# Kernel optimization log

Hardware: AMD Instinct MI355X
Metric: run time of the kernel (lower is better)

Reference implementation:

```python
import jax, jax.numpy as jnp
import numpy as np

N = 4096      # num_nodes
F = 256       # node_dim
K = 4         # num_heads
FP = 64       # out_dim per head
P_EDGE = 0.008  # edge probability (~33 avg degree)


def setup_inputs() -> dict:
    key = jax.random.key(0)
    k1, k2, k3, k4, k5 = jax.random.split(key, 5)
    x = jax.random.normal(k1, (N, F), dtype=jnp.float32)
    # binary adjacency mask with self loops so every row has a neighbor
    adj = (jax.random.uniform(k2, (N, N)) < P_EDGE).astype(jnp.float32)
    mask = jnp.maximum(adj, jnp.eye(N, dtype=jnp.float32))
    batch = jnp.zeros((N,), dtype=jnp.int32)  # unused (is_final_layer=False)
    # xavier-style init for W (node_dim -> K*FP) and attention vectors
    w_scale = np.sqrt(2.0 / (F + K * FP)).astype(np.float32)
    W = jax.random.normal(k3, (F, K * FP), dtype=jnp.float32) * w_scale
    b = jnp.zeros((K * FP,), dtype=jnp.float32)
    a_scale = np.sqrt(2.0 / (K * FP + 1)).astype(np.float32)
    a_left = jax.random.normal(k4, (1, K, FP), dtype=jnp.float32) * a_scale
    a_right = jax.random.normal(k5, (1, K, FP), dtype=jnp.float32) * a_scale
    return {"x": x, "mask": mask, "batch": batch, "W": W, "b": b,
            "a_left": a_left, "a_right": a_right}


def reference(x, mask, batch, W, b, a_left, a_right):
    # dropout prob = 0.0 (eval mode) -> identity
    x_proj = (x @ W + b).reshape(N, K, FP)                 # (N,K,F')
    score_src = (x_proj * a_left).sum(axis=-1)             # (N,K)
    score_tgt = (x_proj * a_right).sum(axis=-1)            # (N,K)
    score = score_src[:, None, :] + score_tgt[None, :, :]  # (N,N,K)
    score = jax.nn.leaky_relu(score, negative_slope=0.2)
    # non-standard global mean/std normalization (torch .std() is unbiased)
    score = (score - score.mean()) / score.std(ddof=1)
    score = jnp.exp(score)
    m = mask[:, :, None]                                   # (N,N,1)
    denom = (score * m).sum(axis=1, keepdims=True)         # (N,1,K)
    aij = (score / denom) * m                              # (N,N,K)
    attention = jnp.transpose(aij, (2, 0, 1))              # (K,N,N)
    h_prime = jnp.einsum('knm,mkf->nkf', attention, x_proj)  # (N,K,F')
    h_prime = jax.nn.elu(h_prime)
    # is_final_layer=False -> concat heads
    return h_prime.reshape(N, K * FP)
```

## Files before the change

kernel.cpp:

```cpp
#include <hip/hip_runtime.h>
#include <hip/hip_bf16.h>
#include <math.h>

#define NN 4096
#define FF 256
#define KH 4
#define FP 64
#define NCOL 256
#define MAXNBR 512
#define GEMM_BLKS 512
#define MOM_BLOCKS 4096

__device__ __forceinline__ float bits2f(unsigned b) {
    union { unsigned u; float f; } c; c.u = b << 16; return c.f;
}
__device__ __forceinline__ int is_fp32(const void* mask) {
    return ((const unsigned*)mask)[0] == 0x3F800000u;
}

#define OFF_PART   0
#define OFF_MUSIG  65536
#define OFF_XP     131072
#define OFF_SRC    4325376
#define OFF_TGT    4390912
#define OFF_NBR    4456448
#define OFF_CNT    8650752

__global__ __launch_bounds__(256) void k_gemm_scan(
        const void* __restrict__ xr, const void* __restrict__ mask,
        const void* __restrict__ Wr, const void* __restrict__ br,
        const void* __restrict__ alr, const void* __restrict__ arr,
        float* __restrict__ xp, float* __restrict__ srcb, float* __restrict__ tgtb,
        unsigned short* __restrict__ nbr_g, int* __restrict__ cnt_g) {
    const int fl = is_fp32(mask);
    const int tid = threadIdx.x;
    __shared__ union {
        float4 xs[8][64];
        struct { unsigned short snbr[MAXNBR]; int cnt; } sc;
    } sm;

    if (blockIdx.x >= GEMM_BLKS) {
        int n = blockIdx.x - GEMM_BLKS;
        if (tid == 0) sm.sc.cnt = 0;
        __syncthreads();
        if (fl) {
            const uint4* p = (const uint4*)((const float*)mask + (size_t)n * NN);
            for (int i = tid; i < NN / 4; i += 256) {
                uint4 v = p[i]; int base = i * 4;
                if (v.x) { int s = atomicAdd(&sm.sc.cnt, 1); if (s < MAXNBR) sm.sc.snbr[s] = base + 0; }
                if (v.y) { int s = atomicAdd(&sm.sc.cnt, 1); if (s < MAXNBR) sm.sc.snbr[s] = base + 1; }
                if (v.z) { int s = atomicAdd(&sm.sc.cnt, 1); if (s < MAXNBR) sm.sc.snbr[s] = base + 2; }
                if (v.w) { int s = atomicAdd(&sm.sc.cnt, 1); if (s < MAXNBR) sm.sc.snbr[s] = base + 3; }
            }
        } else {
            const uint4* p = (const uint4*)((const unsigned short*)mask + (size_t)n * NN);
            for (int i = tid; i < NN / 8; i += 256) {
                uint4 v = p[i]; int base = i * 8;
                if (v.x & 0xFFFFu) { int s = atomicAdd(&sm.sc.cnt, 1); if (s < MAXNBR) sm.sc.snbr[s] = base + 0; }
                if (v.x >> 16)     { int s = atomicAdd(&sm.sc.cnt, 1); if (s < MAXNBR) sm.sc.snbr[s] = base + 1; }
                if (v.y & 0xFFFFu) { int s = atomicAdd(&sm.sc.cnt, 1); if (s < MAXNBR) sm.sc.snbr[s] = base + 2; }
                if (v.y >> 16)     { int s = atomicAdd(&sm.sc.cnt, 1); if (s < MAXNBR) sm.sc.snbr[s] = base + 3; }
                if (v.z & 0xFFFFu) { int s = atomicAdd(&sm.sc.cnt, 1); if (s < MAXNBR) sm.sc.snbr[s] = base + 4; }
                if (v.z >> 16)     { int s = atomicAdd(&sm.sc.cnt, 1); if (s < MAXNBR) sm.sc.snbr[s] = base + 5; }
                if (v.w & 0xFFFFu) { int s = atomicAdd(&sm.sc.cnt, 1); if (s < MAXNBR) sm.sc.snbr[s] = base + 6; }
                if (v.w >> 16)     { int s = atomicAdd(&sm.sc.cnt, 1); if (s < MAXNBR) sm.sc.snbr[s] = base + 7; }
            }
        }
        __syncthreads();
        int c = sm.sc.cnt < MAXNBR ? sm.sc.cnt : MAXNBR;
        for (int j = tid; j < c; j += 256)
            nbr_g[(size_t)n * MAXNBR + j] = sm.sc.snbr[j];
        if (tid == 0) cnt_g[n] = c;
        return;
    }

    int n0 = blockIdx.x * 8;
    if (fl) {
        const float4* xq = (const float4*)xr;
        for (int t = tid; t < 512; t += 256) {
            int r = t >> 6, q = t & 63;
            sm.xs[r][q] = xq[(size_t)(n0 + r) * 64 + q];
        }
    } else {
        const ushort4* xq = (const ushort4*)xr;
        for (int t = tid; t < 512; t += 256) {
            int r = t >> 6, q = t & 63;
            ushort4 u = xq[(size_t)(n0 + r) * 64 + q];
            float4 v; v.x = bits2f(u.x); v.y = bits2f(u.y); v.z = bits2f(u.z); v.w = bits2f(u.w);
            sm.xs[r][q] = v;
        }
    }
    __syncthreads();
    int c = tid;
    float acc[8] = {};
    if (fl) {
        const float* WF = (const float*)Wr;
        for (int kk = 0; kk < 64; ++kk) {
            float w0 = WF[(4 * kk + 0) * NCOL + c];
            float w1 = WF[(4 * kk + 1) * NCOL + c];
            float w2 = WF[(4 * kk + 2) * NCOL + c];
            float w3 = WF[(4 * kk + 3) * NCOL + c];
            #pragma unroll
            for (int r = 0; r < 8; ++r) {
                float4 xv = sm.xs[r][kk];
                acc[r] += xv.x * w0 + xv.y * w1 + xv.z * w2 + xv.w * w3;
            }
        }
    } else {
        const unsigned short* WB = (const unsigned short*)Wr;
        for (int kk = 0; kk < 64; ++kk) {
            float w0 = bits2f(WB[(4 * kk + 0) * NCOL + c]);
            float w1 = bits2f(WB[(4 * kk + 1) * NCOL + c]);
            float w2 = bits2f(WB[(4 * kk + 2) * NCOL + c]);
            float w3 = bits2f(WB[(4 * kk + 3) * NCOL + c]);
            #pragma unroll
            for (int r = 0; r < 8; ++r) {
                float4 xv = sm.xs[r][kk];
                acc[r] += xv.x * w0 + xv.y * w1 + xv.z * w2 + xv.w * w3;
            }
        }
    }
    float bv, alv, arv;
    if (fl) {
        bv  = ((const float*)br)[c];
        alv = ((const float*)alr)[c];
        arv = ((const float*)arr)[c];
    } else {
        bv  = bits2f(((const unsigned short*)br)[c]);
        alv = bits2f(((const unsigned short*)alr)[c]);
        arv = bits2f(((const unsigned short*)arr)[c]);
    }
    int wave = tid >> 6;
    int lane = tid & 63;
    #pragma unroll
    for (int r = 0; r < 8; ++r) {
        float o = acc[r] + bv;
        xp[(size_t)(n0 + r) * NCOL + c] = o;
        float sr = o * alv, tr = o * arv;
        #pragma unroll
        for (int off = 32; off; off >>= 1) {
            sr += __shfl_down(sr, off, 64);
            tr += __shfl_down(tr, off, 64);
        }
        if (lane == 0) {
            srcb[(n0 + r) * KH + wave] = sr;
            tgtb[(n0 + r) * KH + wave] = tr;
        }
    }
}

__global__ __launch_bounds__(256) void k_moments(
        const float* __restrict__ srcb, const float* __restrict__ tgtb,
        double2* __restrict__ partials) {
    const int total = NN * NN;
    const int stride = MOM_BLOCKS * 256;
    float s1 = 0.f, s2 = 0.f;
    #pragma unroll 4
    for (int p = blockIdx.x * 256 + threadIdx.x; p < total; p += stride) {
        int n = p >> 12, m = p & 4095;
        float4 sv = ((const float4*)srcb)[n];
        float4 tv = ((const float4*)tgtb)[m];
        float v0 = sv.x + tv.x; v0 = v0 > 0.f ? v0 : 0.2f * v0;
        float v1 = sv.y + tv.y; v1 = v1 > 0.f ? v1 : 0.2f * v1;
        float v2 = sv.z + tv.z; v2 = v2 > 0.f ? v2 : 0.2f * v2;
        float v3 = sv.w + tv.w; v3 = v3 > 0.f ? v3 : 0.2f * v3;
        s1 += v0 + v1 + v2 + v3;
        s2 += v0 * v0 + v1 * v1 + v2 * v2 + v3 * v3;
    }
    __shared__ double l1[256], l2[256];
    l1[threadIdx.x] = (double)s1;
    l2[threadIdx.x] = (double)s2;
    __syncthreads();
    for (int off = 128; off; off >>= 1) {
        if (threadIdx.x < off) {
            l1[threadIdx.x] += l1[threadIdx.x + off];
            l2[threadIdx.x] += l2[threadIdx.x + off];
        }
        __syncthreads();
    }
    if (threadIdx.x == 0) {
        double2 pr; pr.x = l1[0]; pr.y = l2[0];
        partials[blockIdx.x] = pr;
    }
}

__global__ __launch_bounds__(256) void k_fold(
        const double2* __restrict__ partials, float* __restrict__ musig) {
    double a = 0.0, b2 = 0.0;
    for (int i = threadIdx.x; i < MOM_BLOCKS; i += 256) {
        double2 pr = partials[i];
        a += pr.x; b2 += pr.y;
    }
    __shared__ double l1[256], l2[256];
    l1[threadIdx.x] = a;
    l2[threadIdx.x] = b2;
    __syncthreads();
    for (int off = 128; off; off >>= 1) {
        if (threadIdx.x < off) {
            l1[threadIdx.x] += l1[threadIdx.x + off];
            l2[threadIdx.x] += l2[threadIdx.x + off];
        }
        __syncthreads();
    }
    if (threadIdx.x == 0) {
        double s = l1[0], ss = l2[0];
        const double tot = (double)NN * (double)NN * (double)KH;
        musig[0] = (float)(s / tot);
        musig[1] = (float)(1.0 / sqrt((ss - s * s / tot) / (tot - 1.0)));
    }
}

__global__ __launch_bounds__(256) void k_aggregate(
        const unsigned short* __restrict__ nbr_g, const int* __restrict__ cnt_g,
        const float* __restrict__ musig,
        const float* __restrict__ xp,
        const float* __restrict__ srcb, const float* __restrict__ tgtb,
        float* __restrict__ out) {
    const int tid = threadIdx.x;
    __shared__ unsigned short snbr[MAXNBR];
    __shared__ float pls[MAXNBR * KH];
    __shared__ float invden[KH];
    float mu = musig[0], inv_sigma = musig[1];
    int n = blockIdx.x;
    int c = cnt_g[n];
    for (int j = tid; j < c; j += 256) snbr[j] = nbr_g[(size_t)n * MAXNBR + j];
    __syncthreads();

    for (int t = tid; t < c * KH; t += 256) {
        int j = t >> 2, k = t & 3;
        int m = snbr[j];
        float v = srcb[n * KH + k] + tgtb[m * KH + k];
        v = v > 0.f ? v : 0.2f * v;
        pls[j * KH + k] = expf((v - mu) * inv_sigma);
    }
    __syncthreads();
    if (tid < KH) {
        float d = 0.f;
        for (int j = 0; j < c; ++j) d += pls[j * KH + tid];
        invden[tid] = 1.0f / d;
    }
    __syncthreads();

    int col = tid;
    int k = col >> 6;
    float acc = 0.f;
    for (int j = 0; j < c; ++j) {
        acc += pls[j * KH + k] * xp[(size_t)snbr[j] * NCOL + col];
    }
    acc *= invden[k];
    float o = acc > 0.f ? acc : expm1f(acc);
    out[(size_t)n * NCOL + col] = o;
}

extern "C" void kernel_launch(void* const* d_in, const int* in_sizes, int n_in,
                              void* d_out, int out_size, void* d_ws, size_t ws_size,
                              hipStream_t stream) {
    const void* x    = d_in[0];
    const void* mask = d_in[1];
    const void* W    = d_in[3];
    const void* b    = d_in[4];
    const void* al   = d_in[5];
    const void* ar   = d_in[6];

    char* ws = (char*)d_ws;
    double2* part = (double2*)(ws + OFF_PART);
    float* musig = (float*)(ws + OFF_MUSIG);
    float* xp   = (float*)(ws + OFF_XP);
    float* src  = (float*)(ws + OFF_SRC);
    float* tgt  = (float*)(ws + OFF_TGT);
    unsigned short* nbr = (unsigned short*)(ws + OFF_NBR);
    int* cntg = (int*)(ws + OFF_CNT);

    k_gemm_scan<<<GEMM_BLKS + NN, 256, 0, stream>>>(x, mask, W, b, al, ar,
                                                    xp, src, tgt, nbr, cntg);
    k_moments<<<MOM_BLOCKS, 256, 0, stream>>>(src, tgt, part);
    k_fold<<<1, 256, 0, stream>>>(part, musig);
    k_aggregate<<<NN, 256, 0, stream>>>(nbr, cntg, musig, xp, src, tgt,
                                        (float*)d_out);
}
```

Measured before the change: 157.7 us.

## Split neighbor aggregation across waves with float4 loads and parallel denominator reduction

The aggregation kernel now assigns each of the four waves a strided subset of neighbors. Each lane loads a float4 of the projected features, two neighbors per iteration, and the per-wave partial sums are combined through shared memory. The softmax denominator is computed by a wave-level shuffle reduction instead of four serial threads. The aim is more memory-level parallelism and wider loads per neighbor row, in exchange for an extra shared-memory reduction stage and only 64 threads active in the epilogue.

```diff
diff --git a/kernel.cpp b/kernel.cpp
--- a/kernel.cpp
+++ b/kernel.cpp
@@ -217,9 +217,11 @@
         const float* __restrict__ srcb, const float* __restrict__ tgtb,
         float* __restrict__ out) {
     const int tid = threadIdx.x;
+    const int wave = tid >> 6, lane = tid & 63;
     __shared__ unsigned short snbr[MAXNBR];
     __shared__ float pls[MAXNBR * KH];
     __shared__ float invden[KH];
+    __shared__ float4 red[4][64];
     float mu = musig[0], inv_sigma = musig[1];
     int n = blockIdx.x;
     int c = cnt_g[n];
@@ -231,25 +233,56 @@
         int m = snbr[j];
         float v = srcb[n * KH + k] + tgtb[m * KH + k];
         v = v > 0.f ? v : 0.2f * v;
-        pls[j * KH + k] = expf((v - mu) * inv_sigma);
-    }
-    __syncthreads();
-    if (tid < KH) {
+        pls[t] = expf((v - mu) * inv_sigma);
+    }
+    __syncthreads();
+
+    {
         float d = 0.f;
-        for (int j = 0; j < c; ++j) d += pls[j * KH + tid];
-        invden[tid] = 1.0f / d;
-    }
-    __syncthreads();
-
-    int col = tid;
-    int k = col >> 6;
-    float acc = 0.f;
-    for (int j = 0; j < c; ++j) {
-        acc += pls[j * KH + k] * xp[(size_t)snbr[j] * NCOL + col];
-    }
-    acc *= invden[k];
-    float o = acc > 0.f ? acc : expm1f(acc);
-    out[(size_t)n * NCOL + col] = o;
+        for (int j = lane; j < c; j += 64) d += pls[j * KH + wave];
+        #pragma unroll
+        for (int off = 32; off; off >>= 1) d += __shfl_down(d, off, 64);
+        if (lane == 0) invden[wave] = 1.0f / d;
+    }
+    __syncthreads();
+
+    const int k = lane >> 4;
+    const float4* xp4 = (const float4*)xp;
+    float4 acc = make_float4(0.f, 0.f, 0.f, 0.f);
+    int j = wave;
+    for (; j + 4 < c; j += 8) {
+        int m0 = snbr[j], m1 = snbr[j + 4];
+        float w0 = pls[j * KH + k], w1 = pls[(j + 4) * KH + k];
+        float4 a = xp4[(size_t)m0 * 64 + lane];
+        float4 b = xp4[(size_t)m1 * 64 + lane];
+        acc.x += w0 * a.x + w1 * b.x;
+        acc.y += w0 * a.y + w1 * b.y;
+        acc.z += w0 * a.z + w1 * b.z;
+        acc.w += w0 * a.w + w1 * b.w;
+    }
+    if (j < c) {
+        int m0 = snbr[j];
+        float w0 = pls[j * KH + k];
+        float4 a = xp4[(size_t)m0 * 64 + lane];
+        acc.x += w0 * a.x; acc.y += w0 * a.y;
+        acc.z += w0 * a.z; acc.w += w0 * a.w;
+    }
+    red[wave][lane] = acc;
+    __syncthreads();
+    if (tid < 64) {
+        float4 r0 = red[0][tid], r1 = red[1][tid], r2 = red[2][tid], r3 = red[3][tid];
+        float s = invden[tid >> 4];
+        float4 o;
+        o.x = (r0.x + r1.x + r2.x + r3.x) * s;
+        o.y = (r0.y + r1.y + r2.y + r3.y) * s;
+        o.z = (r0.z + r1.z + r2.z + r3.z) * s;
+        o.w = (r0.w + r1.w + r2.w + r3.w) * s;
+        o.x = o.x > 0.f ? o.x : expm1f(o.x);
+        o.y = o.y > 0.f ? o.y : expm1f(o.y);
+        o.z = o.z > 0.f ? o.z : expm1f(o.z);
+        o.w = o.w > 0.f ? o.w : expm1f(o.w);
+        ((float4*)out)[(size_t)n * 64 + tid] = o;
+    }
 }
 
 extern "C" void kernel_launch(void* const* d_in, const int* in_sizes, int n_in,
```

Result: no change. 156.8 us (-0.6%).
